# Kernel optimization log

Hardware: AMD Instinct MI355X
Metric: run time of the kernel (lower is better)

Reference implementation:

```python
import jax, jax.numpy as jnp
import numpy as np

N_NODES = 60
N_EDGES = 1800
BATCH = 8192
NEG_SLOPE = 0.2  # PyG GATConv default leaky_relu slope


def _conv2d(x, w, b):
    y = jax.lax.conv_general_dilated(x, w, window_strides=(1, 1), padding='VALID',
                                     dimension_numbers=('NCHW', 'OIHW', 'NCHW'))
    return y + b[None, :, None, None]


def _maxpool2(x):
    return jax.lax.reduce_window(x, -jnp.inf, jax.lax.max, (1, 1, 2, 2), (1, 1, 2, 2), 'VALID')


def _gat(x, src, dst, edge_attr, W, a_src, a_dst, We, a_edge, b, n):
    # PyG GATConv, heads=1: xl = x W ; alpha_e = leakyrelu(a_src.xl[src] + a_dst.xl[dst] + a_edge.(edge_attr We))
    xl = x @ W                                    # [N, out]
    asrc = (xl * a_src).sum(-1)                   # [N]
    adst = (xl * a_dst).sum(-1)                   # [N]
    aedge = ((edge_attr @ We) * a_edge).sum(-1)   # [E]
    alpha = jax.nn.leaky_relu(asrc[src] + adst[dst] + aedge, NEG_SLOPE)
    # softmax over incoming edges of each dst node
    m = jax.ops.segment_max(alpha, dst, num_segments=n)
    ex = jnp.exp(alpha - m[dst])
    denom = jax.ops.segment_sum(ex, dst, num_segments=n)
    w_e = ex / denom[dst]
    out = jax.ops.segment_sum(w_e[:, None] * xl[src], dst, num_segments=n)
    return out + b


def _batchnorm_gnn(x):
    # torch code uses .item(): mean/std are detached python floats
    avg = jax.lax.stop_gradient(x.mean())
    std = jax.lax.stop_gradient(jnp.sqrt(((x - avg) ** 2).mean()))
    return (x - avg) / std


def setup_inputs() -> dict:
    key = jax.random.key(0)
    ks = jax.random.split(key, 24)
    f = lambda k, shape, scale=0.1: (jax.random.normal(k, shape, dtype=jnp.float32) * scale)
    inp = {
        'node_fea': jax.random.normal(ks[0], (N_NODES, 1), dtype=jnp.float32),
        'edge_fea': jax.random.normal(ks[1], (N_EDGES, 1), dtype=jnp.float32),
        'pic_fea': jax.random.normal(ks[2], (BATCH, 3, 32, 32), dtype=jnp.float32),
        'conv1_w': f(ks[3], (6, 3, 5, 5)), 'conv1_b': f(ks[4], (6,)),
        'conv2_w': f(ks[5], (16, 6, 5, 5)), 'conv2_b': f(ks[6], (16,)),
        'gat1_w': f(ks[7], (1, 6), 0.5), 'gat1_att_src': f(ks[8], (6,), 0.5),
        'gat1_att_dst': f(ks[9], (6,), 0.5), 'gat1_lin_edge': f(ks[10], (1, 6), 0.5),
        'gat1_att_edge': f(ks[11], (6,), 0.5), 'gat1_b': f(ks[12], (6,)),
        'gat2_w': f(ks[13], (6, 16), 0.3), 'gat2_att_src': f(ks[14], (16,), 0.3),
        'gat2_att_dst': f(ks[15], (16,), 0.3), 'gat2_lin_edge': f(ks[16], (1, 16), 0.3),
        'gat2_att_edge': f(ks[17], (16,), 0.3), 'gat2_b': f(ks[18], (16,)),
        'fc1_w': f(ks[19], (1360, 512), 0.03), 'fc1_b': f(ks[20], (512,)),
        'fc2_w': f(ks[21], (512, 10), 0.05), 'fc2_b': f(ks[22], (10,)),
        'edge_index': jax.random.randint(ks[23], (2, N_EDGES), 0, N_NODES, dtype=jnp.int64 if jax.config.jax_enable_x64 else jnp.int32),
    }
    return inp


def reference(node_fea, edge_fea, pic_fea,
              conv1_w, conv1_b, conv2_w, conv2_b,
              gat1_w, gat1_att_src, gat1_att_dst, gat1_lin_edge, gat1_att_edge, gat1_b,
              gat2_w, gat2_att_src, gat2_att_dst, gat2_lin_edge, gat2_att_edge, gat2_b,
              fc1_w, fc1_b, fc2_w, fc2_b, edge_index):
    n = node_fea.shape[0]
    # CNN branch: 32 -> 28 -> 14 -> 10 -> 5
    p = _maxpool2(jax.nn.relu(_conv2d(pic_fea, conv1_w, conv1_b)))
    p = _maxpool2(jax.nn.relu(_conv2d(p, conv2_w, conv2_b)))
    p = p.reshape(p.shape[0], -1)  # [B, 400]
    # add self loops (PyG default, fill_value='mean' for edge_attr)
    loop = jnp.arange(n)
    src = jnp.concatenate([edge_index[0], loop])
    dst = jnp.concatenate([edge_index[1], loop])
    ea = jnp.concatenate([edge_fea, jnp.broadcast_to(edge_fea.mean(0, keepdims=True), (n, edge_fea.shape[1]))], axis=0)
    # GNN branch
    x = _gat(node_fea, src, dst, ea, gat1_w, gat1_att_src, gat1_att_dst, gat1_lin_edge, gat1_att_edge, gat1_b, n)
    x = jax.nn.relu(_batchnorm_gnn(x))
    x = _gat(x, src, dst, ea, gat2_w, gat2_att_src, gat2_att_dst, gat2_lin_edge, gat2_att_edge, gat2_b, n)
    x = jax.nn.relu(_batchnorm_gnn(x))
    g = x.reshape(-1)  # [960]
    feat = jnp.concatenate([jnp.broadcast_to(g, (p.shape[0], g.shape[0])), p], axis=1)  # [B, 1360]
    h = jax.nn.relu(feat @ fc1_w + fc1_b)
    return jnp.tanh(h @ fc2_w + fc2_b)
```

## Files before the change

kernel.cpp:

```cpp
#include <hip/hip_runtime.h>
#include <math.h>

#define N_NODES 60
#define N_EDGES 1800
#define N_ETOT  1860
#define SLOPE   0.2f

#define SROW 34
#define SCH  (32 * SROW)
#define CROW 16
#define CCH  (14 * CROW)
struct ConvS {
    float simg[3 * SCH];
    float sw1[456], sb1[8];
    float sw2[2400], sb2[16];
    float c1[6 * CCH];
    float pad[8];
};
struct GnnS {
    float alpha[N_ETOT];
    float x_in[960];
    float xl[960];
    float as_[N_NODES], ad_[N_NODES], den_[N_NODES];
    float red[256];
    unsigned char srcs[N_ETOT], dsts[N_ETOT];
    unsigned short csr[N_ETOT];
    int cnt[N_NODES], off[N_NODES + 4];
};
union SMem { ConvS c; GnnS g; };

__device__ __forceinline__ void block_reduce_sum(float v, float* red, float* out) {
    int tid = threadIdx.x;
    red[tid] = v;
    __syncthreads();
    for (int st = 128; st > 0; st >>= 1) {
        if (tid < st) red[tid] += red[tid + st];
        __syncthreads();
    }
    *out = red[0];
    __syncthreads();
}

__device__ void gat_layer(GnnS& S, const float* x_in, int in_dim, int out_dim,
                          const float* W, const float* a_src, const float* a_dst,
                          const float* We, const float* a_edge, const float* bias,
                          const float* edge_fea, float emean,
                          float* xl, float* outb) {
    const int tid = threadIdx.x, nt = blockDim.x;
    for (int idx = tid; idx < N_NODES * out_dim; idx += nt) {
        int i = idx / out_dim, j = idx % out_dim;
        float s = 0.f;
        for (int k = 0; k < in_dim; ++k) s += x_in[i * in_dim + k] * W[k * out_dim + j];
        xl[idx] = s;
    }
    __syncthreads();
    for (int i = tid; i < N_NODES; i += nt) {
        float s = 0.f, d = 0.f;
        for (int j = 0; j < out_dim; ++j) {
            s += xl[i * out_dim + j] * a_src[j];
            d += xl[i * out_dim + j] * a_dst[j];
        }
        S.as_[i] = s; S.ad_[i] = d;
    }
    float ecoef = 0.f;
    for (int j = 0; j < out_dim; ++j) ecoef += We[j] * a_edge[j];
    __syncthreads();
    for (int e = tid; e < N_ETOT; e += nt) {
        float eaval = (e < N_EDGES) ? edge_fea[e] : emean;
        float a = S.as_[S.srcs[e]] + S.ad_[S.dsts[e]] + eaval * ecoef;
        S.alpha[e] = (a >= 0.f) ? a : SLOPE * a;
    }
    __syncthreads();
    for (int d = tid; d < N_NODES; d += nt) {
        float m = -INFINITY;
        for (int k = S.off[d]; k < S.off[d + 1]; ++k) m = fmaxf(m, S.alpha[S.csr[k]]);
        float den = 0.f;
        for (int k = S.off[d]; k < S.off[d + 1]; ++k) {
            int e = S.csr[k];
            float ex = expf(S.alpha[e] - m);
            S.alpha[e] = ex;
            den += ex;
        }
        S.den_[d] = den;
    }
    __syncthreads();
    for (int idx = tid; idx < N_NODES * out_dim; idx += nt) {
        int d = idx / out_dim, j = idx % out_dim;
        float s = 0.f;
        for (int k = S.off[d]; k < S.off[d + 1]; ++k) {
            int e = S.csr[k];
            s += S.alpha[e] * xl[(int)S.srcs[e] * out_dim + j];
        }
        outb[idx] = s / S.den_[d] + bias[j];
    }
    __syncthreads();
}

__device__ void bn_relu(GnnS& S, float* v, int n) {
    const int tid = threadIdx.x, nt = blockDim.x;
    float s = 0.f;
    for (int i = tid; i < n; i += nt) s += v[i];
    float tot;
    block_reduce_sum(s, S.red, &tot);
    float avg = tot / n;
    float s2 = 0.f;
    for (int i = tid; i < n; i += nt) { float d = v[i] - avg; s2 += d * d; }
    block_reduce_sum(s2, S.red, &tot);
    float stdv = sqrtf(tot / n);
    __syncthreads();
    for (int i = tid; i < n; i += nt) v[i] = fmaxf((v[i] - avg) / stdv, 0.f);
    __syncthreads();
}

__device__ void gnn_path(GnnS& S,
    const float* node_fea, const float* edge_fea, const int* eidx,
    const float* g1w, const float* g1as, const float* g1ad,
    const float* g1we, const float* g1ae, const float* g1b,
    const float* g2w, const float* g2as, const float* g2ad,
    const float* g2we, const float* g2ae, const float* g2b,
    const float* fc1w, const float* fc1b, float* gcontrib) {
    const int tid = threadIdx.x, nt = blockDim.x;
    float s = 0.f;
    for (int e = tid; e < N_EDGES; e += nt) s += edge_fea[e];
    float tot;
    block_reduce_sum(s, S.red, &tot);
    float emean = tot / N_EDGES;
    for (int e = tid; e < N_ETOT; e += nt) {
        if (e < N_EDGES) {
            S.srcs[e] = (unsigned char)eidx[e];
            S.dsts[e] = (unsigned char)eidx[N_EDGES + e];
        } else {
            S.srcs[e] = (unsigned char)(e - N_EDGES);
            S.dsts[e] = (unsigned char)(e - N_EDGES);
        }
    }
    if (tid < N_NODES) S.x_in[tid] = node_fea[tid];
    __syncthreads();
    if (tid < N_NODES) {
        int c = 0;
        for (int e = 0; e < N_ETOT; ++e) c += (S.dsts[e] == tid);
        S.cnt[tid] = c;
    }
    __syncthreads();
    if (tid == 0) {
        S.off[0] = 0;
        for (int d = 0; d < N_NODES; ++d) S.off[d + 1] = S.off[d] + S.cnt[d];
    }
    __syncthreads();
    if (tid < N_NODES) {
        int k = S.off[tid];
        for (int e = 0; e < N_ETOT; ++e)
            if (S.dsts[e] == tid) S.csr[k++] = (unsigned short)e;
    }
    __syncthreads();

    gat_layer(S, S.x_in, 1, 6, g1w, g1as, g1ad, g1we, g1ae, g1b,
              edge_fea, emean, S.xl, S.x_in);
    bn_relu(S, S.x_in, N_NODES * 6);
    gat_layer(S, S.x_in, 6, 16, g2w, g2as, g2ad, g2we, g2ae, g2b,
              edge_fea, emean, S.xl, S.x_in);
    bn_relu(S, S.x_in, N_NODES * 16);

    for (int j = tid; j < 512; j += nt) {
        float acc = fc1b[j];
#pragma unroll 4
        for (int k = 0; k < 960; ++k) acc += S.x_in[k] * fc1w[(size_t)k * 512 + j];
        gcontrib[j] = acc;
    }
}

__device__ void conv_path(ConvS& C, int img,
                          const float* __restrict__ pic,
                          const float* __restrict__ w1, const float* __restrict__ b1,
                          const float* __restrict__ w2, const float* __restrict__ b2,
                          float* __restrict__ p) {
    const int tid = threadIdx.x;

    for (int i = tid; i < 768; i += 256) {
        float4 v = ((const float4*)(pic + (size_t)img * 3072))[i];
        int e = 4 * i, ic = e >> 10, rem = e & 1023, y = rem >> 5, x = rem & 31;
        float2* dst = (float2*)&C.simg[ic * SCH + y * SROW + x];
        dst[0] = make_float2(v.x, v.y);
        dst[1] = make_float2(v.z, v.w);
    }
    for (int i = tid; i < 450; i += 256) C.sw1[i] = w1[i];
    if (tid < 6) C.sb1[tid] = b1[tid];
    for (int i = tid; i < 2400; i += 256) C.sw2[i] = w2[i];
    if (tid < 16) C.sb2[tid] = b2[tid];
    __syncthreads();

    for (int it = tid; it < 588; it += 256) {
        int py = it / 42, r = it % 42, oc = r / 7, qx = r % 7;
        int y0 = 2 * py, x0 = 4 * qx;
        float bias = C.sb1[oc];
        float acc[2][4];
#pragma unroll
        for (int dy = 0; dy < 2; ++dy)
#pragma unroll
            for (int dx = 0; dx < 4; ++dx) acc[dy][dx] = bias;

#pragma unroll 1
        for (int ic = 0; ic < 3; ++ic) {
            float wr[25];
#pragma unroll
            for (int k = 0; k < 25; ++k) wr[k] = C.sw1[oc * 75 + ic * 25 + k];
            const float* B = &C.simg[ic * SCH + y0 * SROW + x0];
#pragma unroll
            for (int i = 0; i < 6; ++i) {
                const float2* rp = (const float2*)(B + i * SROW);
                float2 A = rp[0], Bv = rp[1], Cv = rp[2], Dv = rp[3];
                float row[8] = {A.x, A.y, Bv.x, Bv.y, Cv.x, Cv.y, Dv.x, Dv.y};
#pragma unroll
                for (int dy = 0; dy < 2; ++dy) {
                    int ky = i - dy;
                    if (ky >= 0 && ky < 5) {
#pragma unroll
                        for (int dx = 0; dx < 4; ++dx) {
                            float s = 0.f;
#pragma unroll
                            for (int kx = 0; kx < 5; ++kx)
                                s += row[dx + kx] * wr[ky * 5 + kx];
                            acc[dy][dx] += s;
                        }
                    }
                }
            }
        }
#pragma unroll
        for (int sx = 0; sx < 2; ++sx) {
            float m = fmaxf(fmaxf(acc[0][2 * sx], acc[0][2 * sx + 1]),
                            fmaxf(acc[1][2 * sx], acc[1][2 * sx + 1]));
            C.c1[oc * CCH + py * CROW + 2 * qx + sx] = fmaxf(m, 0.f);
        }
    }
    __syncthreads();

    if (tid < 240) {
        int py = tid / 48, r = tid % 48, oc = r / 3, g = r % 3;
        int y0 = 2 * py, x0 = 4 * g;
        float bias = C.sb2[oc];
        float acc[2][4];
#pragma unroll
        for (int dy = 0; dy < 2; ++dy)
#pragma unroll
            for (int dx = 0; dx < 4; ++dx) acc[dy][dx] = bias;

#pragma unroll 1
        for (int ic = 0; ic < 6; ++ic) {
            float wr[25];
#pragma unroll
            for (int k = 0; k < 25; ++k) wr[k] = C.sw2[oc * 150 + ic * 25 + k];
            const float* B = &C.c1[ic * CCH + y0 * CROW + x0];
#pragma unroll
            for (int i = 0; i < 6; ++i) {
                const float2* rp = (const float2*)(B + i * CROW);
                float2 A = rp[0], Bv = rp[1], Cv = rp[2], Dv = rp[3];
                float row[8] = {A.x, A.y, Bv.x, Bv.y, Cv.x, Cv.y, Dv.x, Dv.y};
#pragma unroll
                for (int dy = 0; dy < 2; ++dy) {
                    int ky = i - dy;
                    if (ky >= 0 && ky < 5) {
#pragma unroll
                        for (int dx = 0; dx < 4; ++dx) {
                            float s = 0.f;
#pragma unroll
                            for (int kx = 0; kx < 5; ++kx)
                                s += row[dx + kx] * wr[ky * 5 + kx];
                            acc[dy][dx] += s;
                        }
                    }
                }
            }
        }
        float m0 = fmaxf(fmaxf(acc[0][0], acc[0][1]), fmaxf(acc[1][0], acc[1][1]));
        float m1 = fmaxf(fmaxf(acc[0][2], acc[0][3]), fmaxf(acc[1][2], acc[1][3]));
        float* prow = p + ((size_t)img * 16 + oc) * 25 + py * 5;
        prow[2 * g] = fmaxf(m0, 0.f);
        if (g < 2) prow[2 * g + 1] = fmaxf(m1, 0.f);
    }
}

__global__ void __launch_bounds__(256, 5) fused_kernel(
    const float* __restrict__ node_fea, const float* __restrict__ edge_fea,
    const int* __restrict__ eidx,
    const float* g1w, const float* g1as, const float* g1ad,
    const float* g1we, const float* g1ae, const float* g1b,
    const float* g2w, const float* g2as, const float* g2ad,
    const float* g2we, const float* g2ae, const float* g2b,
    const float* __restrict__ fc1w, const float* __restrict__ fc1b,
    float* __restrict__ gcontrib,
    const float* __restrict__ pic,
    const float* __restrict__ c1w, const float* __restrict__ c1b,
    const float* __restrict__ c2w, const float* __restrict__ c2b,
    float* __restrict__ p) {
    __shared__ SMem u;
    if (blockIdx.x == 0) {
        gnn_path(u.g, node_fea, edge_fea, eidx,
                 g1w, g1as, g1ad, g1we, g1ae, g1b,
                 g2w, g2as, g2ad, g2we, g2ae, g2b,
                 fc1w, fc1b, gcontrib);
    } else {
        conv_path(u.c, blockIdx.x - 1, pic, c1w, c1b, c2w, c2b, p);
    }
}

#define FC1_ROWS 16
__global__ void fc1_kernel(
    const float* __restrict__ p, const float* __restrict__ w,
    const float* __restrict__ gcontrib, float* __restrict__ h) {
    __shared__ float sp[FC1_ROWS * 400];
    const int tid = threadIdx.x;
    const size_t r0 = (size_t)blockIdx.x * FC1_ROWS;
    for (int i = tid; i < FC1_ROWS * 400; i += 256) sp[i] = p[r0 * 400 + i];
    __syncthreads();
    const int c0 = tid, c1 = tid + 256;
    float acc[FC1_ROWS][2];
#pragma unroll
    for (int r = 0; r < FC1_ROWS; ++r) { acc[r][0] = 0.f; acc[r][1] = 0.f; }
    for (int k = 0; k < 400; k += 4) {
        float wa0 = w[(size_t)(k + 0) * 512 + c0], wa1 = w[(size_t)(k + 0) * 512 + c1];
        float wb0 = w[(size_t)(k + 1) * 512 + c0], wb1 = w[(size_t)(k + 1) * 512 + c1];
        float wc0 = w[(size_t)(k + 2) * 512 + c0], wc1 = w[(size_t)(k + 2) * 512 + c1];
        float wd0 = w[(size_t)(k + 3) * 512 + c0], wd1 = w[(size_t)(k + 3) * 512 + c1];
#pragma unroll
        for (int r = 0; r < FC1_ROWS; ++r) {
            float4 pv = *(const float4*)&sp[r * 400 + k];
            acc[r][0] += pv.x * wa0 + pv.y * wb0 + pv.z * wc0 + pv.w * wd0;
            acc[r][1] += pv.x * wa1 + pv.y * wb1 + pv.z * wc1 + pv.w * wd1;
        }
    }
    float g0 = gcontrib[c0], g1 = gcontrib[c1];
#pragma unroll
    for (int r = 0; r < FC1_ROWS; ++r) {
        h[(r0 + r) * 512 + c0] = fmaxf(acc[r][0] + g0, 0.f);
        h[(r0 + r) * 512 + c1] = fmaxf(acc[r][1] + g1, 0.f);
    }
}

__global__ void fc2_kernel(
    const float* __restrict__ h, const float* __restrict__ w,
    const float* __restrict__ b, float* __restrict__ out) {
    const int wave = threadIdx.x >> 6, lane = threadIdx.x & 63;
    const size_t row = (size_t)blockIdx.x * 4 + wave;
    const float* hr = h + row * 512;
    float partial[10];
#pragma unroll
    for (int j = 0; j < 10; ++j) partial[j] = 0.f;
    for (int k = lane; k < 512; k += 64) {
        float hv = hr[k];
        const float* wr = w + (size_t)k * 10;
#pragma unroll
        for (int j = 0; j < 10; ++j) partial[j] += hv * wr[j];
    }
#pragma unroll
    for (int j = 0; j < 10; ++j) {
        float v = partial[j];
        for (int sft = 32; sft > 0; sft >>= 1) v += __shfl_xor(v, sft, 64);
        partial[j] = v;
    }
    if (lane == 0) {
#pragma unroll
        for (int j = 0; j < 10; ++j)
            out[row * 10 + j] = tanhf(partial[j] + b[j]);
    }
}

extern "C" void kernel_launch(void* const* d_in, const int* in_sizes, int n_in,
                              void* d_out, int out_size, void* d_ws, size_t ws_size,
                              hipStream_t stream) {
    const float* node_fea = (const float*)d_in[0];
    const float* edge_fea = (const float*)d_in[1];
    const float* pic      = (const float*)d_in[2];
    const float* c1w = (const float*)d_in[3];
    const float* c1b = (const float*)d_in[4];
    const float* c2w = (const float*)d_in[5];
    const float* c2b = (const float*)d_in[6];
    const float* g1w  = (const float*)d_in[7];
    const float* g1as = (const float*)d_in[8];
    const float* g1ad = (const float*)d_in[9];
    const float* g1we = (const float*)d_in[10];
    const float* g1ae = (const float*)d_in[11];
    const float* g1b  = (const float*)d_in[12];
    const float* g2w  = (const float*)d_in[13];
    const float* g2as = (const float*)d_in[14];
    const float* g2ad = (const float*)d_in[15];
    const float* g2we = (const float*)d_in[16];
    const float* g2ae = (const float*)d_in[17];
    const float* g2b  = (const float*)d_in[18];
    const float* fc1w = (const float*)d_in[19];
    const float* fc1b = (const float*)d_in[20];
    const float* fc2w = (const float*)d_in[21];
    const float* fc2b = (const float*)d_in[22];
    const int*   eidx = (const int*)d_in[23];
    float* out = (float*)d_out;

    char* ws = (char*)d_ws;
    float* gcontrib = (float*)ws;
    float* p = (float*)(ws + 2048);
    float* h = (float*)(ws + 2048 + (size_t)8192 * 400 * 4);

    hipLaunchKernelGGL(fused_kernel, dim3(8193), dim3(256), 0, stream,
                       node_fea, edge_fea, eidx,
                       g1w, g1as, g1ad, g1we, g1ae, g1b,
                       g2w, g2as, g2ad, g2we, g2ae, g2b,
                       fc1w, fc1b, gcontrib,
                       pic, c1w, c1b, c2w, c2b, p);
    hipLaunchKernelGGL(fc1_kernel, dim3(8192 / FC1_ROWS), dim3(256), 0, stream,
                       p, fc1w + (size_t)960 * 512, gcontrib, h);
    hipLaunchKernelGGL(fc2_kernel, dim3(8192 / 4), dim3(256), 0, stream,
                       h, fc2w, fc2b, out);
}
```

Baseline: 456.3 us.

## Shrink shared memory by reading conv1 input from global and moving GNN scratch out

Drops the staged input image from shared memory so conv1 reads pic directly from global memory with float4 loads. The large GNN scratch arrays (alpha, features, edge lists, CSR) move to a global workspace, so the shared-memory union gets much smaller and launch bounds rise from 5 to 7 blocks per CU. Thread-to-output mappings are also permuted so adjacent threads share input pixels, and the c1 row pitch changes. The aim is higher occupancy, at the cost of conv1 input reads going through cache rather than LDS and slower global-memory scratch in the single GNN block.

```diff
diff --git a/kernel.cpp b/kernel.cpp
--- a/kernel.cpp
+++ b/kernel.cpp
@@ -6,28 +6,19 @@
 #define N_ETOT  1860
 #define SLOPE   0.2f
 
-#define SROW 34
-#define SCH  (32 * SROW)
-#define CROW 16
+#define CROW 18
 #define CCH  (14 * CROW)
 struct ConvS {
-    float simg[3 * SCH];
+    float c1[6 * CCH];
     float sw1[456], sb1[8];
     float sw2[2400], sb2[16];
-    float c1[6 * CCH];
-    float pad[8];
 };
-struct GnnS {
-    float alpha[N_ETOT];
-    float x_in[960];
-    float xl[960];
+struct GnnSmall {
     float as_[N_NODES], ad_[N_NODES], den_[N_NODES];
     float red[256];
-    unsigned char srcs[N_ETOT], dsts[N_ETOT];
-    unsigned short csr[N_ETOT];
     int cnt[N_NODES], off[N_NODES + 4];
 };
-union SMem { ConvS c; GnnS g; };
+union SMem { ConvS c; GnnSmall g; };
 
 __device__ __forceinline__ void block_reduce_sum(float v, float* red, float* out) {
     int tid = threadIdx.x;
@@ -41,11 +32,12 @@
     __syncthreads();
 }
 
-__device__ void gat_layer(GnnS& S, const float* x_in, int in_dim, int out_dim,
+__device__ void gat_layer(GnnSmall& S, const float* x_in, int in_dim, int out_dim,
                           const float* W, const float* a_src, const float* a_dst,
                           const float* We, const float* a_edge, const float* bias,
                           const float* edge_fea, float emean,
-                          float* xl, float* outb) {
+                          const int* gsrcs, const int* gdsts, const int* gcsr,
+                          float* galpha, float* xl, float* outb) {
     const int tid = threadIdx.x, nt = blockDim.x;
     for (int idx = tid; idx < N_NODES * out_dim; idx += nt) {
         int i = idx / out_dim, j = idx % out_dim;
@@ -67,18 +59,18 @@
     __syncthreads();
     for (int e = tid; e < N_ETOT; e += nt) {
         float eaval = (e < N_EDGES) ? edge_fea[e] : emean;
-        float a = S.as_[S.srcs[e]] + S.ad_[S.dsts[e]] + eaval * ecoef;
-        S.alpha[e] = (a >= 0.f) ? a : SLOPE * a;
+        float a = S.as_[gsrcs[e]] + S.ad_[gdsts[e]] + eaval * ecoef;
+        galpha[e] = (a >= 0.f) ? a : SLOPE * a;
     }
     __syncthreads();
     for (int d = tid; d < N_NODES; d += nt) {
         float m = -INFINITY;
-        for (int k = S.off[d]; k < S.off[d + 1]; ++k) m = fmaxf(m, S.alpha[S.csr[k]]);
+        for (int k = S.off[d]; k < S.off[d + 1]; ++k) m = fmaxf(m, galpha[gcsr[k]]);
         float den = 0.f;
         for (int k = S.off[d]; k < S.off[d + 1]; ++k) {
-            int e = S.csr[k];
-            float ex = expf(S.alpha[e] - m);
-            S.alpha[e] = ex;
+            int e = gcsr[k];
+            float ex = expf(galpha[e] - m);
+            galpha[e] = ex;
             den += ex;
         }
         S.den_[d] = den;
@@ -88,15 +80,15 @@
         int d = idx / out_dim, j = idx % out_dim;
         float s = 0.f;
         for (int k = S.off[d]; k < S.off[d + 1]; ++k) {
-            int e = S.csr[k];
-            s += S.alpha[e] * xl[(int)S.srcs[e] * out_dim + j];
+            int e = gcsr[k];
+            s += galpha[e] * xl[gsrcs[e] * out_dim + j];
         }
         outb[idx] = s / S.den_[d] + bias[j];
     }
     __syncthreads();
 }
 
-__device__ void bn_relu(GnnS& S, float* v, int n) {
+__device__ void bn_relu(GnnSmall& S, float* v, int n) {
     const int tid = threadIdx.x, nt = blockDim.x;
     float s = 0.f;
     for (int i = tid; i < n; i += nt) s += v[i];
@@ -112,13 +104,14 @@
     __syncthreads();
 }
 
-__device__ void gnn_path(GnnS& S,
+__device__ void gnn_path(GnnSmall& S,
     const float* node_fea, const float* edge_fea, const int* eidx,
     const float* g1w, const float* g1as, const float* g1ad,
     const float* g1we, const float* g1ae, const float* g1b,
     const float* g2w, const float* g2as, const float* g2ad,
     const float* g2we, const float* g2ae, const float* g2b,
-    const float* fc1w, const float* fc1b, float* gcontrib) {
+    const float* fc1w, const float* fc1b, float* gcontrib,
+    float* galpha, float* gx, float* gxl, int* gsrcs, int* gdsts, int* gcsr) {
     const int tid = threadIdx.x, nt = blockDim.x;
     float s = 0.f;
     for (int e = tid; e < N_EDGES; e += nt) s += edge_fea[e];
@@ -127,18 +120,18 @@
     float emean = tot / N_EDGES;
     for (int e = tid; e < N_ETOT; e += nt) {
         if (e < N_EDGES) {
-            S.srcs[e] = (unsigned char)eidx[e];
-            S.dsts[e] = (unsigned char)eidx[N_EDGES + e];
+            gsrcs[e] = eidx[e];
+            gdsts[e] = eidx[N_EDGES + e];
         } else {
-            S.srcs[e] = (unsigned char)(e - N_EDGES);
-            S.dsts[e] = (unsigned char)(e - N_EDGES);
-        }
-    }
-    if (tid < N_NODES) S.x_in[tid] = node_fea[tid];
+            gsrcs[e] = e - N_EDGES;
+            gdsts[e] = e - N_EDGES;
+        }
+    }
+    if (tid < N_NODES) gx[tid] = node_fea[tid];
     __syncthreads();
     if (tid < N_NODES) {
         int c = 0;
-        for (int e = 0; e < N_ETOT; ++e) c += (S.dsts[e] == tid);
+        for (int e = 0; e < N_ETOT; ++e) c += (gdsts[e] == tid);
         S.cnt[tid] = c;
     }
     __syncthreads();
@@ -150,21 +143,21 @@
     if (tid < N_NODES) {
         int k = S.off[tid];
         for (int e = 0; e < N_ETOT; ++e)
-            if (S.dsts[e] == tid) S.csr[k++] = (unsigned short)e;
-    }
-    __syncthreads();
-
-    gat_layer(S, S.x_in, 1, 6, g1w, g1as, g1ad, g1we, g1ae, g1b,
-              edge_fea, emean, S.xl, S.x_in);
-    bn_relu(S, S.x_in, N_NODES * 6);
-    gat_layer(S, S.x_in, 6, 16, g2w, g2as, g2ad, g2we, g2ae, g2b,
-              edge_fea, emean, S.xl, S.x_in);
-    bn_relu(S, S.x_in, N_NODES * 16);
+            if (gdsts[e] == tid) gcsr[k++] = e;
+    }
+    __syncthreads();
+
+    gat_layer(S, gx, 1, 6, g1w, g1as, g1ad, g1we, g1ae, g1b,
+              edge_fea, emean, gsrcs, gdsts, gcsr, galpha, gxl, gx);
+    bn_relu(S, gx, N_NODES * 6);
+    gat_layer(S, gx, 6, 16, g2w, g2as, g2ad, g2we, g2ae, g2b,
+              edge_fea, emean, gsrcs, gdsts, gcsr, galpha, gxl, gx);
+    bn_relu(S, gx, N_NODES * 16);
 
     for (int j = tid; j < 512; j += nt) {
         float acc = fc1b[j];
 #pragma unroll 4
-        for (int k = 0; k < 960; ++k) acc += S.x_in[k] * fc1w[(size_t)k * 512 + j];
+        for (int k = 0; k < 960; ++k) acc += gx[k] * fc1w[(size_t)k * 512 + j];
         gcontrib[j] = acc;
     }
 }
@@ -176,21 +169,16 @@
                           float* __restrict__ p) {
     const int tid = threadIdx.x;
 
-    for (int i = tid; i < 768; i += 256) {
-        float4 v = ((const float4*)(pic + (size_t)img * 3072))[i];
-        int e = 4 * i, ic = e >> 10, rem = e & 1023, y = rem >> 5, x = rem & 31;
-        float2* dst = (float2*)&C.simg[ic * SCH + y * SROW + x];
-        dst[0] = make_float2(v.x, v.y);
-        dst[1] = make_float2(v.z, v.w);
-    }
     for (int i = tid; i < 450; i += 256) C.sw1[i] = w1[i];
     if (tid < 6) C.sb1[tid] = b1[tid];
     for (int i = tid; i < 2400; i += 256) C.sw2[i] = w2[i];
     if (tid < 16) C.sb2[tid] = b2[tid];
     __syncthreads();
 
+    const float* IMG = pic + (size_t)img * 3072;
+
     for (int it = tid; it < 588; it += 256) {
-        int py = it / 42, r = it % 42, oc = r / 7, qx = r % 7;
+        int py = it / 42, r = it % 42, qx = r / 6, oc = r % 6;
         int y0 = 2 * py, x0 = 4 * qx;
         float bias = C.sb1[oc];
         float acc[2][4];
@@ -204,12 +192,12 @@
             float wr[25];
 #pragma unroll
             for (int k = 0; k < 25; ++k) wr[k] = C.sw1[oc * 75 + ic * 25 + k];
-            const float* B = &C.simg[ic * SCH + y0 * SROW + x0];
+            const float* B = IMG + ic * 1024 + y0 * 32 + x0;
 #pragma unroll
             for (int i = 0; i < 6; ++i) {
-                const float2* rp = (const float2*)(B + i * SROW);
-                float2 A = rp[0], Bv = rp[1], Cv = rp[2], Dv = rp[3];
-                float row[8] = {A.x, A.y, Bv.x, Bv.y, Cv.x, Cv.y, Dv.x, Dv.y};
+                float4 A = *(const float4*)(B + i * 32);
+                float4 Bv = *(const float4*)(B + i * 32 + 4);
+                float row[8] = {A.x, A.y, A.z, A.w, Bv.x, Bv.y, Bv.z, Bv.w};
 #pragma unroll
                 for (int dy = 0; dy < 2; ++dy) {
                     int ky = i - dy;
@@ -236,7 +224,7 @@
     __syncthreads();
 
     if (tid < 240) {
-        int py = tid / 48, r = tid % 48, oc = r / 3, g = r % 3;
+        int py = tid / 48, r = tid % 48, g = r / 16, oc = r % 16;
         int y0 = 2 * py, x0 = 4 * g;
         float bias = C.sb2[oc];
         float acc[2][4];
@@ -280,7 +268,7 @@
     }
 }
 
-__global__ void __launch_bounds__(256, 5) fused_kernel(
+__global__ void __launch_bounds__(256, 7) fused_kernel(
     const float* __restrict__ node_fea, const float* __restrict__ edge_fea,
     const int* __restrict__ eidx,
     const float* g1w, const float* g1as, const float* g1ad,
@@ -292,13 +280,14 @@
     const float* __restrict__ pic,
     const float* __restrict__ c1w, const float* __restrict__ c1b,
     const float* __restrict__ c2w, const float* __restrict__ c2b,
-    float* __restrict__ p) {
+    float* __restrict__ p,
+    float* galpha, float* gx, float* gxl, int* gsrcs, int* gdsts, int* gcsr) {
     __shared__ SMem u;
     if (blockIdx.x == 0) {
         gnn_path(u.g, node_fea, edge_fea, eidx,
                  g1w, g1as, g1ad, g1we, g1ae, g1b,
                  g2w, g2as, g2ad, g2we, g2ae, g2b,
-                 fc1w, fc1b, gcontrib);
+                 fc1w, fc1b, gcontrib, galpha, gx, gxl, gsrcs, gdsts, gcsr);
     } else {
         conv_path(u.c, blockIdx.x - 1, pic, c1w, c1b, c2w, c2b, p);
     }
@@ -398,13 +387,21 @@
     float* gcontrib = (float*)ws;
     float* p = (float*)(ws + 2048);
     float* h = (float*)(ws + 2048 + (size_t)8192 * 400 * 4);
+    char*  gs = ws + 2048 + (size_t)8192 * 400 * 4 + (size_t)8192 * 512 * 4;
+    float* galpha = (float*)gs;
+    float* gx     = (float*)(gs + 7680);
+    float* gxl    = (float*)(gs + 7680 + 3840);
+    int*   gsrcs  = (int*)(gs + 15360);
+    int*   gdsts  = (int*)(gs + 15360 + 7680);
+    int*   gcsr   = (int*)(gs + 15360 + 15360);
 
     hipLaunchKernelGGL(fused_kernel, dim3(8193), dim3(256), 0, stream,
                        node_fea, edge_fea, eidx,
                        g1w, g1as, g1ad, g1we, g1ae, g1b,
                        g2w, g2as, g2ad, g2we, g2ae, g2b,
                        fc1w, fc1b, gcontrib,
-                       pic, c1w, c1b, c2w, c2b, p);
+                       pic, c1w, c1b, c2w, c2b, p,
+                       galpha, gx, gxl, gsrcs, gdsts, gcsr);
     hipLaunchKernelGGL(fc1_kernel, dim3(8192 / FC1_ROWS), dim3(256), 0, stream,
                        p, fc1w + (size_t)960 * 512, gcontrib, h);
     hipLaunchKernelGGL(fc2_kernel, dim3(8192 / 4), dim3(256), 0, stream,
```

Result: slower. 783.4 us (+71.7%).
